# Kernel tuning notes

Hardware: AMD Instinct MI355X
Metric: run time of the kernel (lower is better)

## Reference

```python
import jax, jax.numpy as jnp
import numpy as np

N_NODES = 100000
DEG = 16   # regular-graph degree -> every per-node subgraph is a (DEG+1)-node star
DIM = 128


def _crelu(z):
    return (jax.nn.relu(z.real) + 1j * jax.nn.relu(z.imag)).astype(jnp.complex64)


def _evolution_row(deg, tr, ti):
    # get_node_adjacency keeps only edges incident to the center node, so A_i is the
    # star graph K_{1,deg} with the center at index 0 -- identical for every node of a
    # deg-regular graph, so U is computed once.
    n = deg + 1
    A = jnp.zeros((n, n), jnp.complex64).at[0, 1:].set(1.0).at[1:, 0].set(1.0)
    t = (tr + 1j * ti).astype(jnp.complex64)
    G = jax.scipy.linalg.expm(-1j * A * t)
    # torch: sqrt(max eigval of G G^dagger); G G^dagger is Hermitian PSD -> eigvalsh
    s = jnp.sqrt(jnp.max(jnp.linalg.eigvalsh(G @ G.conj().T))).astype(jnp.complex64)
    Lt = G / s
    # np.sqrt on a matrix is ELEMENTWISE sqrt in the torch code -- replicate that
    Rt = jnp.sqrt(jnp.eye(n, dtype=jnp.complex64) - Lt @ (G.conj().T / s))
    # torch converts complex_time via .item() into numpy: no grad through U
    return jax.lax.stop_gradient(Lt[0] + Rt[0])  # (deg+1,) complex row 0 of [[Lt,Rt],[Rt,-Lt]]


def _layer(h, nbrs, Wr, Wi, br, bi, tr, ti, ebr, ebi):
    W = (Wr + 1j * Wi).astype(jnp.complex64)
    b = (br + 1j * bi).astype(jnp.complex64)
    h = _crelu(h @ W.T + b)
    deg = nbrs.shape[1]
    w = _evolution_row(deg, tr, ti)
    # evolved[0] = w[0]*h_i + sum_k w[1+k]*h_{sorted_nbr_k(i)}
    out = w[0] * h
    for k in range(deg):  # fixed small unrolled loop; avoids a [N, deg+1, C] intermediate
        out = out + w[1 + k] * h[nbrs[:, k]]
    return out + (ebr + 1j * ebi).astype(jnp.complex64)


def setup_inputs():
    key = jax.random.key(0)
    ks = jax.random.split(key, 12)
    x = jax.random.normal(ks[0], (N_NODES, DIM), jnp.float32)
    # circulant DEG-regular graph: node i ~ i +/- k (mod N), k=1..DEG/2; each undirected edge once
    K = DEG // 2
    i = np.arange(N_NODES)
    src = np.repeat(i, K)
    dst = ((i[:, None] + np.arange(1, K + 1)[None, :]) % N_NODES).reshape(-1)
    edge_index = jnp.asarray(np.stack([src, dst]), dtype=jnp.int32)
    sc = 0.05
    d = {"x": x, "edge_index": edge_index}
    for l, k0 in ((1, 1), (2, 6)):
        d[f"W{l}r"] = jax.random.normal(ks[k0], (DIM, DIM), jnp.float32) * sc
        d[f"W{l}i"] = jax.random.normal(ks[k0 + 1], (DIM, DIM), jnp.float32) * sc
        d[f"b{l}r"] = jax.random.normal(ks[k0 + 2], (DIM,), jnp.float32) * sc
        d[f"b{l}i"] = jax.random.normal(ks[k0 + 3], (DIM,), jnp.float32) * sc
        d[f"t{l}r"] = jnp.float32(1.0)
        d[f"t{l}i"] = jnp.float32(0.0)
        d[f"eb{l}r"] = jnp.zeros((DIM,), jnp.float32)
        d[f"eb{l}i"] = jnp.zeros((DIM,), jnp.float32)
    return d


def reference(x, edge_index, W1r, W1i, b1r, b1i, t1r, t1i, eb1r, eb1i,
              W2r, W2i, b2r, b2i, t2r, t2i, eb2r, eb2i):
    N = x.shape[0]
    src, dst = edge_index[0], edge_index[1]
    nodes = jnp.concatenate([src, dst])
    nbr = jnp.concatenate([dst, src])
    order = jnp.lexsort((nbr, nodes))        # sorted neighbor list per node
    deg = nodes.shape[0] // N                # regular graph -> static degree
    nbrs = nbr[order].reshape(N, deg)        # [N, DEG]
    h = x.astype(jnp.complex64)              # prepare_complex_input
    h = _layer(h, nbrs, W1r, W1i, b1r, b1i, t1r, t1i, eb1r, eb1i)
    h = _layer(h, nbrs, W2r, W2i, b2r, b2i, t2r, t2i, eb2r, eb2i)
    return h.real                            # output_type='real'
```

## Files before the change

### kernel.cpp

```cpp
#include <hip/hip_runtime.h>
#include <hip/hip_bf16.h>
#include <stdint.h>

typedef __attribute__((ext_vector_type(8))) short bf8_t;
typedef __attribute__((ext_vector_type(4))) float f32x4_t;
typedef __attribute__((ext_vector_type(4))) unsigned short us4_t;

#define MFMA_BF16 __builtin_amdgcn_mfma_f32_16x16x32_bf16

__device__ __forceinline__ unsigned short f2bf(float f) {
  union { float f; unsigned u; } x; x.f = f;
  unsigned r = (x.u + 0x7FFFu + ((x.u >> 16) & 1u)) >> 16;
  return (unsigned short)r;
}
__device__ __forceinline__ float bf2f(unsigned short b) {
  union { unsigned u; float f; } x; x.u = ((unsigned)b) << 16;
  return x.f;
}

__global__ void compute_wscal(const float* t1r, const float* t1i,
                              const float* t2r, const float* t2i,
                              float* wsc, int deg) {
  if (threadIdx.x != 0 || blockIdx.x != 0) return;
  float r = sqrtf((float)deg);
  for (int l = 0; l < 2; ++l) {
    float tr = l ? t2r[0] : t1r[0];
    float ti = l ? t2i[0] : t1i[0];
    float x = r * tr, y = r * ti;
    float cr = cosf(x) * coshf(y), ci = -sinf(x) * sinhf(y);
    float sr = sinf(x) * coshf(y), si = cosf(x) * sinhf(y);
    float a = cr * cr + ci * ci + sr * sr + si * si;
    float b = -2.0f * (ci * sr - cr * si);
    float s2 = fmaxf(a + fabsf(b), 1.0f);
    float s = sqrtf(s2);
    float l0r = cr / s, l0i = ci / s;
    float l1r = si / (r * s), l1i = -sr / (r * s);
    float q0 = 1.0f - a / s2;
    float r0r = (q0 >= 0.0f) ? sqrtf(q0) : 0.0f;
    float r0i = (q0 >= 0.0f) ? 0.0f : sqrtf(-q0);
    float q1 = -b / (r * s2);
    float r1r = (q1 >= 0.0f) ? sqrtf(q1) : 0.0f;
    float r1i = (q1 >= 0.0f) ? 0.0f : sqrtf(-q1);
    wsc[l * 4 + 0] = l0r + r0r;
    wsc[l * 4 + 1] = l0i + r0i;
    wsc[l * 4 + 2] = l1r + r1r;
    wsc[l * 4 + 3] = l1i + r1i;
  }
}

__global__ __launch_bounds__(256) void build_nbrs(
    const int* __restrict__ ei, int E, int* __restrict__ cnt,
    int* __restrict__ nbrs, int deg) {
  int e = blockIdx.x * 256 + threadIdx.x;
  if (e >= E) return;
  int s = ei[e], d = ei[E + e];
  int p = atomicAdd(&cnt[s], 1); nbrs[(long)s * deg + p] = d;
  int q = atomicAdd(&cnt[d], 1); nbrs[(long)d * deg + q] = s;
}

template <int COMPLEX>
__global__ __launch_bounds__(512) void gemm_fused(
    const float* __restrict__ Xf,
    const unsigned short* __restrict__ Ar, const unsigned short* __restrict__ Ai,
    const float* __restrict__ Wr, const float* __restrict__ Wi,
    const float* __restrict__ br, const float* __restrict__ bi,
    unsigned short* __restrict__ Or, unsigned short* __restrict__ Oi, int n) {
  __shared__ unsigned char ldsW[65536];
  const int tid = threadIdx.x;

#pragma unroll
  for (int p = 0; p < 2; ++p) {
    const float* src = p ? Wi : Wr;
#pragma unroll
    for (int i = 0; i < 4; ++i) {
      const int e8 = (i * 512 + tid) * 8;
      float4 a = *(const float4*)(src + e8);
      float4 b = *(const float4*)(src + e8 + 4);
      union { bf8_t v; unsigned short s[8]; } o;
      o.s[0] = f2bf(a.x); o.s[1] = f2bf(a.y); o.s[2] = f2bf(a.z); o.s[3] = f2bf(a.w);
      o.s[4] = f2bf(b.x); o.s[5] = f2bf(b.y); o.s[6] = f2bf(b.z); o.s[7] = f2bf(b.w);
      const int c = e8 >> 7, k = e8 & 127;
      const int byte = p * 32768 + c * 256 + ((k * 2) ^ ((c & 7) << 4));
      *(bf8_t*)(ldsW + byte) = o.v;
    }
  }
  __syncthreads();

  const int wv = tid >> 6, lane = tid & 63;
  const int fr = lane & 15, kg = lane >> 4;
  const int rowbase = blockIdx.x * 128 + wv * 16;
  const int node = min(rowbase + fr, n - 1);
  const long a_off = (long)node * 128;

  f32x4_t accr[8], acci[8];
#pragma unroll
  for (int i = 0; i < 8; ++i) { accr[i] = (f32x4_t)0.0f; acci[i] = (f32x4_t)0.0f; }

#pragma unroll
  for (int ks = 0; ks < 4; ++ks) {
    const int koff = ks * 32 + kg * 8;
    bf8_t a_r, a_i = {}, a_in = {};
    if (COMPLEX) {
      a_r = *(const bf8_t*)(Ar + a_off + koff);
      a_i = *(const bf8_t*)(Ai + a_off + koff);
      union { bf8_t v; unsigned u[4]; } t;
      t.v = a_i;
#pragma unroll
      for (int q = 0; q < 4; ++q) t.u[q] ^= 0x80008000u;
      a_in = t.v;
    } else {
      float4 u = *(const float4*)(Xf + a_off + koff);
      float4 v = *(const float4*)(Xf + a_off + koff + 4);
      union { bf8_t vv; unsigned short s[8]; } t;
      t.s[0] = f2bf(u.x); t.s[1] = f2bf(u.y); t.s[2] = f2bf(u.z); t.s[3] = f2bf(u.w);
      t.s[4] = f2bf(v.x); t.s[5] = f2bf(v.y); t.s[6] = f2bf(v.z); t.s[7] = f2bf(v.w);
      a_r = t.vv;
    }
#pragma unroll
    for (int cf = 0; cf < 8; ++cf) {
      const int c = cf * 16 + fr;
      const int wbyte = c * 256 + ((koff * 2) ^ ((c & 7) << 4));
      bf8_t w_r = *(const bf8_t*)(ldsW + wbyte);
      bf8_t w_i = *(const bf8_t*)(ldsW + 32768 + wbyte);
      accr[cf] = MFMA_BF16(w_r, a_r, accr[cf], 0, 0, 0);
      acci[cf] = MFMA_BF16(w_i, a_r, acci[cf], 0, 0, 0);
      if (COMPLEX) {
        accr[cf] = MFMA_BF16(w_i, a_in, accr[cf], 0, 0, 0);
        acci[cf] = MFMA_BF16(w_r, a_i, acci[cf], 0, 0, 0);
      }
    }
  }

  const int onode = rowbase + fr;
  if (onode < n) {
    const long obase = (long)onode * 128;
#pragma unroll
    for (int cf = 0; cf < 8; ++cf) {
      const int cb = cf * 16 + kg * 4;
      union { float4 f4; float f[4]; } b4r, b4i;
      b4r.f4 = *(const float4*)(br + cb);
      b4i.f4 = *(const float4*)(bi + cb);
      us4_t pr, pi;
#pragma unroll
      for (int j = 0; j < 4; ++j) {
        pr[j] = f2bf(fmaxf(accr[cf][j] + b4r.f[j], 0.0f));
        pi[j] = f2bf(fmaxf(acci[cf][j] + b4i.f[j], 0.0f));
      }
      *(us4_t*)(Or + obase + cb) = pr;
      *(us4_t*)(Oi + obase + cb) = pi;
    }
  }
}

template <int DEG, int FINAL>
__global__ __launch_bounds__(256) void agg_kernel(
    const unsigned short* __restrict__ hr, const unsigned short* __restrict__ hi,
    const int* __restrict__ nbrs, const float* __restrict__ wsc,
    const float* __restrict__ ebr, const float* __restrict__ ebi,
    unsigned short* __restrict__ outr, unsigned short* __restrict__ outi,
    float* __restrict__ outf, int n, int deg_rt) {
  const int g = blockIdx.x * 256 + threadIdx.x;
  const int node = g >> 4;
  if (node >= n) return;
  const int ch0 = (g & 15) * 8;
  const int deg = DEG ? DEG : deg_rt;
  const float w0r = wsc[0], w0i = wsc[1], w1r = wsc[2], w1i = wsc[3];

  union { bf8_t v; unsigned short s[8]; } ur, ui;
  ur.v = *(const bf8_t*)(hr + (long)node * 128 + ch0);
  ui.v = *(const bf8_t*)(hi + (long)node * 128 + ch0);
  float hrf[8], hif[8], srf[8], sif[8];
#pragma unroll
  for (int e = 0; e < 8; ++e) {
    hrf[e] = bf2f(ur.s[e]); hif[e] = bf2f(ui.s[e]);
    srf[e] = 0.0f; sif[e] = 0.0f;
  }
  const int* nb = nbrs + (long)node * deg;
#pragma unroll
  for (int k = 0; k < (DEG ? DEG : 1); ++k) {
    for (int kk = DEG ? k : 0; kk < (DEG ? k + 1 : deg); ++kk) {
      const long m = (long)nb[kk] * 128 + ch0;
      union { bf8_t v; unsigned short s[8]; } vr2, vi2;
      vr2.v = *(const bf8_t*)(hr + m);
      vi2.v = *(const bf8_t*)(hi + m);
#pragma unroll
      for (int e = 0; e < 8; ++e) {
        srf[e] += bf2f(vr2.s[e]);
        sif[e] += bf2f(vi2.s[e]);
      }
    }
  }
  if (FINAL) {
    union { float4 f4; float f[4]; } o0, o1;
#pragma unroll
    for (int e = 0; e < 8; ++e) {
      const int c = ch0 + e;
      float R = w0r * hrf[e] - w0i * hif[e] + w1r * srf[e] - w1i * sif[e] + ebr[c];
      if (e < 4) o0.f[e] = R; else o1.f[e - 4] = R;
    }
    *(float4*)(outf + (long)node * 128 + ch0) = o0.f4;
    *(float4*)(outf + (long)node * 128 + ch0 + 4) = o1.f4;
  } else {
    union { bf8_t v; unsigned short s[8]; } pr, pi;
#pragma unroll
    for (int e = 0; e < 8; ++e) {
      const int c = ch0 + e;
      float R = w0r * hrf[e] - w0i * hif[e] + w1r * srf[e] - w1i * sif[e] + ebr[c];
      float I = w0r * hif[e] + w0i * hrf[e] + w1r * sif[e] + w1i * srf[e] + ebi[c];
      pr.s[e] = f2bf(R); pi.s[e] = f2bf(I);
    }
    *(bf8_t*)(outr + (long)node * 128 + ch0) = pr.v;
    *(bf8_t*)(outi + (long)node * 128 + ch0) = pi.v;
  }
}

extern "C" void kernel_launch(void* const* d_in, const int* in_sizes, int n_in,
                              void* d_out, int out_size, void* d_ws, size_t ws_size,
                              hipStream_t stream) {
  const float* x    = (const float*)d_in[0];
  const int*   ei   = (const int*)d_in[1];
  const float* W1r  = (const float*)d_in[2];
  const float* W1i  = (const float*)d_in[3];
  const float* b1r  = (const float*)d_in[4];
  const float* b1i  = (const float*)d_in[5];
  const float* t1r  = (const float*)d_in[6];
  const float* t1i  = (const float*)d_in[7];
  const float* eb1r = (const float*)d_in[8];
  const float* eb1i = (const float*)d_in[9];
  const float* W2r  = (const float*)d_in[10];
  const float* W2i  = (const float*)d_in[11];
  const float* b2r  = (const float*)d_in[12];
  const float* b2i  = (const float*)d_in[13];
  const float* t2r  = (const float*)d_in[14];
  const float* t2i  = (const float*)d_in[15];
  const float* eb2r = (const float*)d_in[16];
  const float* eb2i = (const float*)d_in[17];

  const int DIM = 128;
  const int N = in_sizes[0] / DIM;
  const int E = in_sizes[1] / 2;
  const int deg = (2 * E) / N;

  char* ws = (char*)d_ws;
  size_t off = 0;
  auto alloc = [&](size_t bytes) -> char* {
    char* p = ws + off;
    off += (bytes + 255) & ~(size_t)255;
    return p;
  };
  int* cnt  = (int*)alloc((size_t)N * 4);
  int* nbrs = (int*)alloc((size_t)N * deg * 4);
  float* wsc = (float*)alloc(8 * 4);
  const size_t nH = (size_t)N * DIM;
  unsigned short* h1r = (unsigned short*)alloc(nH * 2);
  unsigned short* h1i = (unsigned short*)alloc(nH * 2);
  unsigned short* g1r = (unsigned short*)alloc(nH * 2);
  unsigned short* g1i = (unsigned short*)alloc(nH * 2);
  (void)ws_size; (void)n_in; (void)out_size;

  hipMemsetAsync(cnt, 0, (size_t)N * 4, stream);
  build_nbrs<<<(E + 255) / 256, 256, 0, stream>>>(ei, E, cnt, nbrs, deg);
  compute_wscal<<<1, 64, 0, stream>>>(t1r, t1i, t2r, t2i, wsc, deg);

  const int gemm_blocks = (N + 127) / 128;
  const int agg_blocks = (N * 16 + 255) / 256;

  gemm_fused<0><<<gemm_blocks, 512, 0, stream>>>(x, nullptr, nullptr, W1r, W1i,
                                                 b1r, b1i, h1r, h1i, N);
  if (deg == 16) {
    agg_kernel<16, 0><<<agg_blocks, 256, 0, stream>>>(h1r, h1i, nbrs, wsc, eb1r, eb1i,
                                                      g1r, g1i, nullptr, N, deg);
  } else {
    agg_kernel<0, 0><<<agg_blocks, 256, 0, stream>>>(h1r, h1i, nbrs, wsc, eb1r, eb1i,
                                                     g1r, g1i, nullptr, N, deg);
  }
  gemm_fused<1><<<gemm_blocks, 512, 0, stream>>>(nullptr, g1r, g1i, W2r, W2i,
                                                 b2r, b2i, h1r, h1i, N);
  if (deg == 16) {
    agg_kernel<16, 1><<<agg_blocks, 256, 0, stream>>>(h1r, h1i, nbrs, wsc + 4, eb2r, eb2i,
                                                      nullptr, nullptr, (float*)d_out, N, deg);
  } else {
    agg_kernel<0, 1><<<agg_blocks, 256, 0, stream>>>(h1r, h1i, nbrs, wsc + 4, eb2r, eb2i,
                                                     nullptr, nullptr, (float*)d_out, N, deg);
  }
}
```

Baseline: 347.0 us.

## Fuse layer-1 aggregation into layer-2 GEMM and aggregate atomics per wavefront

The layer-1 neighbor aggregation is moved into the prologue of the layer-2 GEMM, so the aggregated features are built in registers as MFMA operands and the g1 round trip through global memory goes away. The GEMMs are restructured to loop over column fragments with a single accumulator pair each, which lowers register pressure. build_nbrs now groups lanes by key and issues one atomicAdd per distinct key per wavefront. The trade-off is that the fused kernel does a register-heavy 16-neighbor gather with 512-thread blocks, which may limit occupancy and latency hiding.

```diff
diff --git a/kernel.cpp b/kernel.cpp
--- a/kernel.cpp
+++ b/kernel.cpp
@@ -48,26 +48,40 @@
   }
 }
 
+__device__ __forceinline__ void store_side(int* __restrict__ cnt,
+                                           int* __restrict__ nbrs,
+                                           int deg, int key, int val) {
+  unsigned long long remaining = __ballot(1);
+  unsigned long long mymask = 0;
+  while (remaining) {
+    int lead = __ffsll((long long)remaining) - 1;
+    int lkey = __shfl(key, lead);
+    unsigned long long m = __ballot(key == lkey);
+    if (key == lkey) mymask = m;
+    remaining &= ~m;
+  }
+  const int lane = threadIdx.x & 63;
+  const int leader = __ffsll((long long)mymask) - 1;
+  int base = 0;
+  if (lane == leader) base = atomicAdd(&cnt[key], __popcll(mymask));
+  base = __shfl(base, leader);
+  const int rank = __popcll(mymask & ((1ull << lane) - 1ull));
+  nbrs[(long)key * deg + base + rank] = val;
+}
+
 __global__ __launch_bounds__(256) void build_nbrs(
     const int* __restrict__ ei, int E, int* __restrict__ cnt,
     int* __restrict__ nbrs, int deg) {
   int e = blockIdx.x * 256 + threadIdx.x;
   if (e >= E) return;
   int s = ei[e], d = ei[E + e];
-  int p = atomicAdd(&cnt[s], 1); nbrs[(long)s * deg + p] = d;
-  int q = atomicAdd(&cnt[d], 1); nbrs[(long)d * deg + q] = s;
-}
-
-template <int COMPLEX>
-__global__ __launch_bounds__(512) void gemm_fused(
-    const float* __restrict__ Xf,
-    const unsigned short* __restrict__ Ar, const unsigned short* __restrict__ Ai,
-    const float* __restrict__ Wr, const float* __restrict__ Wi,
-    const float* __restrict__ br, const float* __restrict__ bi,
-    unsigned short* __restrict__ Or, unsigned short* __restrict__ Oi, int n) {
-  __shared__ unsigned char ldsW[65536];
-  const int tid = threadIdx.x;
-
+  store_side(cnt, nbrs, deg, s, d);
+  store_side(cnt, nbrs, deg, d, s);
+}
+
+__device__ __forceinline__ void stage_w(unsigned char* ldsW,
+                                        const float* __restrict__ Wr,
+                                        const float* __restrict__ Wi, int tid) {
 #pragma unroll
   for (int p = 0; p < 2; ++p) {
     const float* src = p ? Wi : Wr;
@@ -84,6 +98,16 @@
       *(bf8_t*)(ldsW + byte) = o.v;
     }
   }
+}
+
+__global__ __launch_bounds__(512) void gemm_l1(
+    const float* __restrict__ Xf,
+    const float* __restrict__ Wr, const float* __restrict__ Wi,
+    const float* __restrict__ br, const float* __restrict__ bi,
+    unsigned short* __restrict__ Or, unsigned short* __restrict__ Oi, int n) {
+  __shared__ unsigned char ldsW[65536];
+  const int tid = threadIdx.x;
+  stage_w(ldsW, Wr, Wi, tid);
   __syncthreads();
 
   const int wv = tid >> 6, lane = tid & 63;
@@ -92,50 +116,34 @@
   const int node = min(rowbase + fr, n - 1);
   const long a_off = (long)node * 128;
 
-  f32x4_t accr[8], acci[8];
-#pragma unroll
-  for (int i = 0; i < 8; ++i) { accr[i] = (f32x4_t)0.0f; acci[i] = (f32x4_t)0.0f; }
-
+  bf8_t a[4];
 #pragma unroll
   for (int ks = 0; ks < 4; ++ks) {
     const int koff = ks * 32 + kg * 8;
-    bf8_t a_r, a_i = {}, a_in = {};
-    if (COMPLEX) {
-      a_r = *(const bf8_t*)(Ar + a_off + koff);
-      a_i = *(const bf8_t*)(Ai + a_off + koff);
-      union { bf8_t v; unsigned u[4]; } t;
-      t.v = a_i;
-#pragma unroll
-      for (int q = 0; q < 4; ++q) t.u[q] ^= 0x80008000u;
-      a_in = t.v;
-    } else {
-      float4 u = *(const float4*)(Xf + a_off + koff);
-      float4 v = *(const float4*)(Xf + a_off + koff + 4);
-      union { bf8_t vv; unsigned short s[8]; } t;
-      t.s[0] = f2bf(u.x); t.s[1] = f2bf(u.y); t.s[2] = f2bf(u.z); t.s[3] = f2bf(u.w);
-      t.s[4] = f2bf(v.x); t.s[5] = f2bf(v.y); t.s[6] = f2bf(v.z); t.s[7] = f2bf(v.w);
-      a_r = t.vv;
-    }
-#pragma unroll
-    for (int cf = 0; cf < 8; ++cf) {
-      const int c = cf * 16 + fr;
-      const int wbyte = c * 256 + ((koff * 2) ^ ((c & 7) << 4));
-      bf8_t w_r = *(const bf8_t*)(ldsW + wbyte);
-      bf8_t w_i = *(const bf8_t*)(ldsW + 32768 + wbyte);
-      accr[cf] = MFMA_BF16(w_r, a_r, accr[cf], 0, 0, 0);
-      acci[cf] = MFMA_BF16(w_i, a_r, acci[cf], 0, 0, 0);
-      if (COMPLEX) {
-        accr[cf] = MFMA_BF16(w_i, a_in, accr[cf], 0, 0, 0);
-        acci[cf] = MFMA_BF16(w_r, a_i, acci[cf], 0, 0, 0);
-      }
-    }
+    float4 u = *(const float4*)(Xf + a_off + koff);
+    float4 v = *(const float4*)(Xf + a_off + koff + 4);
+    union { bf8_t vv; unsigned short s[8]; } t;
+    t.s[0] = f2bf(u.x); t.s[1] = f2bf(u.y); t.s[2] = f2bf(u.z); t.s[3] = f2bf(u.w);
+    t.s[4] = f2bf(v.x); t.s[5] = f2bf(v.y); t.s[6] = f2bf(v.z); t.s[7] = f2bf(v.w);
+    a[ks] = t.vv;
   }
 
   const int onode = rowbase + fr;
-  if (onode < n) {
-    const long obase = (long)onode * 128;
-#pragma unroll
-    for (int cf = 0; cf < 8; ++cf) {
+  const long obase = (long)onode * 128;
+#pragma unroll
+  for (int cf = 0; cf < 8; ++cf) {
+    const int c = cf * 16 + fr;
+    const int cbyte = c * 256, swz = (c & 7) << 4;
+    f32x4_t accr = (f32x4_t)0.0f, acci = (f32x4_t)0.0f;
+#pragma unroll
+    for (int ks = 0; ks < 4; ++ks) {
+      const int kb = (ks * 32 + kg * 8) * 2;
+      bf8_t w_r = *(const bf8_t*)(ldsW + cbyte + (kb ^ swz));
+      bf8_t w_i = *(const bf8_t*)(ldsW + 32768 + cbyte + (kb ^ swz));
+      accr = MFMA_BF16(w_r, a[ks], accr, 0, 0, 0);
+      acci = MFMA_BF16(w_i, a[ks], acci, 0, 0, 0);
+    }
+    if (onode < n) {
       const int cb = cf * 16 + kg * 4;
       union { float4 f4; float f[4]; } b4r, b4i;
       b4r.f4 = *(const float4*)(br + cb);
@@ -143,8 +151,8 @@
       us4_t pr, pi;
 #pragma unroll
       for (int j = 0; j < 4; ++j) {
-        pr[j] = f2bf(fmaxf(accr[cf][j] + b4r.f[j], 0.0f));
-        pi[j] = f2bf(fmaxf(acci[cf][j] + b4i.f[j], 0.0f));
+        pr[j] = f2bf(fmaxf(accr[j] + b4r.f[j], 0.0f));
+        pi[j] = f2bf(fmaxf(acci[j] + b4i.f[j], 0.0f));
       }
       *(us4_t*)(Or + obase + cb) = pr;
       *(us4_t*)(Oi + obase + cb) = pi;
@@ -152,12 +160,126 @@
   }
 }
 
-template <int DEG, int FINAL>
-__global__ __launch_bounds__(256) void agg_kernel(
+template <int DEG>
+__global__ __launch_bounds__(512) void fused_l2(
+    const unsigned short* __restrict__ h1r, const unsigned short* __restrict__ h1i,
+    const int* __restrict__ nbrs, const float* __restrict__ wsc,
+    const float* __restrict__ eb1r, const float* __restrict__ eb1i,
+    const float* __restrict__ W2r, const float* __restrict__ W2i,
+    const float* __restrict__ b2r, const float* __restrict__ b2i,
+    unsigned short* __restrict__ Or, unsigned short* __restrict__ Oi,
+    int n, int deg_rt) {
+  __shared__ unsigned char ldsW[65536];
+  const int tid = threadIdx.x;
+  stage_w(ldsW, W2r, W2i, tid);
+  __syncthreads();
+
+  const int wv = tid >> 6, lane = tid & 63;
+  const int fr = lane & 15, kg = lane >> 4;
+  const int rowbase = blockIdx.x * 128 + wv * 16;
+  const int node = min(rowbase + fr, n - 1);
+  const long a_off = (long)node * 128;
+  const float w0r = wsc[0], w0i = wsc[1], w1r = wsc[2], w1i = wsc[3];
+  const int deg = DEG ? DEG : deg_rt;
+  const int* nbp = nbrs + (long)node * deg;
+
+  int nb[DEG ? DEG : 1];
+  if (DEG) {
+#pragma unroll
+    for (int j = 0; j < (DEG ? DEG : 1); ++j) nb[j] = nbp[j];
+  }
+
+  bf8_t ar[4], ai[4], ain[4];
+#pragma unroll
+  for (int ks = 0; ks < 4; ++ks) {
+    const int koff = ks * 32 + kg * 8;
+    union { bf8_t v; unsigned short s[8]; } o_r, o_i;
+    o_r.v = *(const bf8_t*)(h1r + a_off + koff);
+    o_i.v = *(const bf8_t*)(h1i + a_off + koff);
+    float sr[8], si[8];
+#pragma unroll
+    for (int e = 0; e < 8; ++e) { sr[e] = 0.0f; si[e] = 0.0f; }
+    if (DEG) {
+#pragma unroll
+      for (int j = 0; j < (DEG ? DEG : 1); ++j) {
+        const long m = (long)nb[j] * 128 + koff;
+        union { bf8_t v; unsigned short s[8]; } vr2, vi2;
+        vr2.v = *(const bf8_t*)(h1r + m);
+        vi2.v = *(const bf8_t*)(h1i + m);
+#pragma unroll
+        for (int e = 0; e < 8; ++e) { sr[e] += bf2f(vr2.s[e]); si[e] += bf2f(vi2.s[e]); }
+      }
+    } else {
+      for (int j = 0; j < deg; ++j) {
+        const long m = (long)nbp[j] * 128 + koff;
+        union { bf8_t v; unsigned short s[8]; } vr2, vi2;
+        vr2.v = *(const bf8_t*)(h1r + m);
+        vi2.v = *(const bf8_t*)(h1i + m);
+#pragma unroll
+        for (int e = 0; e < 8; ++e) { sr[e] += bf2f(vr2.s[e]); si[e] += bf2f(vi2.s[e]); }
+      }
+    }
+    union { float4 f4; float f[4]; } er0, er1, ei0, ei1;
+    er0.f4 = *(const float4*)(eb1r + koff);
+    er1.f4 = *(const float4*)(eb1r + koff + 4);
+    ei0.f4 = *(const float4*)(eb1i + koff);
+    ei1.f4 = *(const float4*)(eb1i + koff + 4);
+    union { bf8_t v; unsigned short s[8]; } pr, pi;
+#pragma unroll
+    for (int e = 0; e < 8; ++e) {
+      float hr = bf2f(o_r.s[e]), hi = bf2f(o_i.s[e]);
+      float ebR = (e < 4) ? er0.f[e] : er1.f[e - 4];
+      float ebI = (e < 4) ? ei0.f[e] : ei1.f[e - 4];
+      float gr = w0r * hr - w0i * hi + w1r * sr[e] - w1i * si[e] + ebR;
+      float gi = w0r * hi + w0i * hr + w1r * si[e] + w1i * sr[e] + ebI;
+      pr.s[e] = f2bf(gr); pi.s[e] = f2bf(gi);
+    }
+    ar[ks] = pr.v; ai[ks] = pi.v;
+    union { bf8_t v; unsigned u[4]; } t; t.v = pi.v;
+#pragma unroll
+    for (int q = 0; q < 4; ++q) t.u[q] ^= 0x80008000u;
+    ain[ks] = t.v;
+  }
+
+  const int onode = rowbase + fr;
+  const long obase = (long)onode * 128;
+#pragma unroll
+  for (int cf = 0; cf < 8; ++cf) {
+    const int c = cf * 16 + fr;
+    const int cbyte = c * 256, swz = (c & 7) << 4;
+    f32x4_t accr = (f32x4_t)0.0f, acci = (f32x4_t)0.0f;
+#pragma unroll
+    for (int ks = 0; ks < 4; ++ks) {
+      const int kb = (ks * 32 + kg * 8) * 2;
+      bf8_t w_r = *(const bf8_t*)(ldsW + cbyte + (kb ^ swz));
+      bf8_t w_i = *(const bf8_t*)(ldsW + 32768 + cbyte + (kb ^ swz));
+      accr = MFMA_BF16(w_r, ar[ks], accr, 0, 0, 0);
+      accr = MFMA_BF16(w_i, ain[ks], accr, 0, 0, 0);
+      acci = MFMA_BF16(w_i, ar[ks], acci, 0, 0, 0);
+      acci = MFMA_BF16(w_r, ai[ks], acci, 0, 0, 0);
+    }
+    if (onode < n) {
+      const int cb = cf * 16 + kg * 4;
+      union { float4 f4; float f[4]; } b4r, b4i;
+      b4r.f4 = *(const float4*)(b2r + cb);
+      b4i.f4 = *(const float4*)(b2i + cb);
+      us4_t pr, pi;
+#pragma unroll
+      for (int j = 0; j < 4; ++j) {
+        pr[j] = f2bf(fmaxf(accr[j] + b4r.f[j], 0.0f));
+        pi[j] = f2bf(fmaxf(acci[j] + b4i.f[j], 0.0f));
+      }
+      *(us4_t*)(Or + obase + cb) = pr;
+      *(us4_t*)(Oi + obase + cb) = pi;
+    }
+  }
+}
+
+template <int DEG>
+__global__ __launch_bounds__(256) void agg_final(
     const unsigned short* __restrict__ hr, const unsigned short* __restrict__ hi,
     const int* __restrict__ nbrs, const float* __restrict__ wsc,
-    const float* __restrict__ ebr, const float* __restrict__ ebi,
-    unsigned short* __restrict__ outr, unsigned short* __restrict__ outi,
+    const float* __restrict__ ebr,
     float* __restrict__ outf, int n, int deg_rt) {
   const int g = blockIdx.x * 256 + threadIdx.x;
   const int node = g >> 4;
@@ -169,49 +291,40 @@
   union { bf8_t v; unsigned short s[8]; } ur, ui;
   ur.v = *(const bf8_t*)(hr + (long)node * 128 + ch0);
   ui.v = *(const bf8_t*)(hi + (long)node * 128 + ch0);
-  float hrf[8], hif[8], srf[8], sif[8];
-#pragma unroll
-  for (int e = 0; e < 8; ++e) {
-    hrf[e] = bf2f(ur.s[e]); hif[e] = bf2f(ui.s[e]);
-    srf[e] = 0.0f; sif[e] = 0.0f;
-  }
-  const int* nb = nbrs + (long)node * deg;
-#pragma unroll
-  for (int k = 0; k < (DEG ? DEG : 1); ++k) {
-    for (int kk = DEG ? k : 0; kk < (DEG ? k + 1 : deg); ++kk) {
-      const long m = (long)nb[kk] * 128 + ch0;
+  float srf[8], sif[8];
+#pragma unroll
+  for (int e = 0; e < 8; ++e) { srf[e] = 0.0f; sif[e] = 0.0f; }
+  const int* nbp = nbrs + (long)node * deg;
+  if (DEG) {
+#pragma unroll
+    for (int k = 0; k < (DEG ? DEG : 1); ++k) {
+      const long m = (long)nbp[k] * 128 + ch0;
       union { bf8_t v; unsigned short s[8]; } vr2, vi2;
       vr2.v = *(const bf8_t*)(hr + m);
       vi2.v = *(const bf8_t*)(hi + m);
 #pragma unroll
-      for (int e = 0; e < 8; ++e) {
-        srf[e] += bf2f(vr2.s[e]);
-        sif[e] += bf2f(vi2.s[e]);
-      }
-    }
-  }
-  if (FINAL) {
-    union { float4 f4; float f[4]; } o0, o1;
-#pragma unroll
-    for (int e = 0; e < 8; ++e) {
-      const int c = ch0 + e;
-      float R = w0r * hrf[e] - w0i * hif[e] + w1r * srf[e] - w1i * sif[e] + ebr[c];
-      if (e < 4) o0.f[e] = R; else o1.f[e - 4] = R;
-    }
-    *(float4*)(outf + (long)node * 128 + ch0) = o0.f4;
-    *(float4*)(outf + (long)node * 128 + ch0 + 4) = o1.f4;
+      for (int e = 0; e < 8; ++e) { srf[e] += bf2f(vr2.s[e]); sif[e] += bf2f(vi2.s[e]); }
+    }
   } else {
-    union { bf8_t v; unsigned short s[8]; } pr, pi;
-#pragma unroll
-    for (int e = 0; e < 8; ++e) {
-      const int c = ch0 + e;
-      float R = w0r * hrf[e] - w0i * hif[e] + w1r * srf[e] - w1i * sif[e] + ebr[c];
-      float I = w0r * hif[e] + w0i * hrf[e] + w1r * sif[e] + w1i * srf[e] + ebi[c];
-      pr.s[e] = f2bf(R); pi.s[e] = f2bf(I);
-    }
-    *(bf8_t*)(outr + (long)node * 128 + ch0) = pr.v;
-    *(bf8_t*)(outi + (long)node * 128 + ch0) = pi.v;
-  }
+    for (int k = 0; k < deg; ++k) {
+      const long m = (long)nbp[k] * 128 + ch0;
+      union { bf8_t v; unsigned short s[8]; } vr2, vi2;
+      vr2.v = *(const bf8_t*)(hr + m);
+      vi2.v = *(const bf8_t*)(hi + m);
+#pragma unroll
+      for (int e = 0; e < 8; ++e) { srf[e] += bf2f(vr2.s[e]); sif[e] += bf2f(vi2.s[e]); }
+    }
+  }
+  union { float4 f4; float f[4]; } o0, o1;
+#pragma unroll
+  for (int e = 0; e < 8; ++e) {
+    const int c = ch0 + e;
+    float hrf = bf2f(ur.s[e]), hif = bf2f(ui.s[e]);
+    float R = w0r * hrf - w0i * hif + w1r * srf[e] - w1i * sif[e] + ebr[c];
+    if (e < 4) o0.f[e] = R; else o1.f[e - 4] = R;
+  }
+  *(float4*)(outf + (long)node * 128 + ch0) = o0.f4;
+  *(float4*)(outf + (long)node * 128 + ch0 + 4) = o1.f4;
 }
 
 extern "C" void kernel_launch(void* const* d_in, const int* in_sizes, int n_in,
@@ -254,8 +367,8 @@
   const size_t nH = (size_t)N * DIM;
   unsigned short* h1r = (unsigned short*)alloc(nH * 2);
   unsigned short* h1i = (unsigned short*)alloc(nH * 2);
-  unsigned short* g1r = (unsigned short*)alloc(nH * 2);
-  unsigned short* g1i = (unsigned short*)alloc(nH * 2);
+  unsigned short* h2r = (unsigned short*)alloc(nH * 2);
+  unsigned short* h2i = (unsigned short*)alloc(nH * 2);
   (void)ws_size; (void)n_in; (void)out_size;
 
   hipMemsetAsync(cnt, 0, (size_t)N * 4, stream);
@@ -265,22 +378,17 @@
   const int gemm_blocks = (N + 127) / 128;
   const int agg_blocks = (N * 16 + 255) / 256;
 
-  gemm_fused<0><<<gemm_blocks, 512, 0, stream>>>(x, nullptr, nullptr, W1r, W1i,
-                                                 b1r, b1i, h1r, h1i, N);
+  gemm_l1<<<gemm_blocks, 512, 0, stream>>>(x, W1r, W1i, b1r, b1i, h1r, h1i, N);
+
   if (deg == 16) {
-    agg_kernel<16, 0><<<agg_blocks, 256, 0, stream>>>(h1r, h1i, nbrs, wsc, eb1r, eb1i,
-                                                      g1r, g1i, nullptr, N, deg);
+    fused_l2<16><<<gemm_blocks, 512, 0, stream>>>(h1r, h1i, nbrs, wsc, eb1r, eb1i,
+                                                  W2r, W2i, b2r, b2i, h2r, h2i, N, deg);
+    agg_final<16><<<agg_blocks, 256, 0, stream>>>(h2r, h2i, nbrs, wsc + 4, eb2r,
+                                                  (float*)d_out, N, deg);
   } else {
-    agg_kernel<0, 0><<<agg_blocks, 256, 0, stream>>>(h1r, h1i, nbrs, wsc, eb1r, eb1i,
-                                                     g1r, g1i, nullptr, N, deg);
-  }
-  gemm_fused<1><<<gemm_blocks, 512, 0, stream>>>(nullptr, g1r, g1i, W2r, W2i,
-                                                 b2r, b2i, h1r, h1i, N);
-  if (deg == 16) {
-    agg_kernel<16, 1><<<agg_blocks, 256, 0, stream>>>(h1r, h1i, nbrs, wsc + 4, eb2r, eb2i,
-                                                      nullptr, nullptr, (float*)d_out, N, deg);
-  } else {
-    agg_kernel<0, 1><<<agg_blocks, 256, 0, stream>>>(h1r, h1i, nbrs, wsc + 4, eb2r, eb2i,
-                                                     nullptr, nullptr, (float*)d_out, N, deg);
-  }
-}
+    fused_l2<0><<<gemm_blocks, 512, 0, stream>>>(h1r, h1i, nbrs, wsc, eb1r, eb1i,
+                                                 W2r, W2i, b2r, b2i, h2r, h2i, N, deg);
+    agg_final<0><<<agg_blocks, 256, 0, stream>>>(h2r, h2i, nbrs, wsc + 4, eb2r,
+                                                 (float*)d_out, N, deg);
+  }
+}
```

Result: slower. 400.3 us (+15.4%).
